# Performance work log

Hardware: AMD Instinct MI355X
Metric: run time of the kernel (lower is better)

The kernel has to match this reference:

```python
import jax, jax.numpy as jnp
import numpy as np

B, N, E, T, DIN, H, G, ND, NT, L = 4, 10000, 320000, 16, 16, 64, 64, 16, 3, 7


def _mlp2(x, W1, b1, W2, b2):
    # Linear -> LeakyReLU -> (Dropout: eval identity) -> Linear -> LeakyReLU
    h = jax.nn.leaky_relu(x @ W1 + b1)
    return jax.nn.leaky_relu(h @ W2 + b2)


def _gcn_conv(x, src, dst, ew, nt, W1, b1, W2, b2):
    # x: [B,N,D], nt: [B,N,ND], ew: [*,E,1] broadcastable over batch
    x_in = _mlp2(jnp.concatenate([x, nt], axis=-1), W1, b1, W2, b2)  # [B,N,G]
    msgs = x_in[:, src, :] * ew                                      # gather + weight, [B,E,G]
    aggr = jnp.zeros(x_in.shape, x_in.dtype).at[:, dst, :].add(msgs) # scatter-add, [B,N,G]
    return x + aggr


def _gru(x, Wx, Wh, bx, bh):
    # PyTorch-style GRU over time axis. x: [B,N,T,DIN] -> hs: [T,B,N,H]
    xw = jnp.einsum('bntd,dh->tbnh', x, Wx) + bx  # precompute input projections [T,B,N,3H]
    h0 = jnp.zeros(x.shape[:2] + (Wh.shape[0],), x.dtype)

    def step(h, xw_t):
        hw = h @ Wh + bh
        xr, xz, xn = jnp.split(xw_t, 3, axis=-1)
        hr, hz, hn = jnp.split(hw, 3, axis=-1)
        r = jax.nn.sigmoid(xr + hr)
        z = jax.nn.sigmoid(xz + hz)
        n = jnp.tanh(xn + r * hn)
        h_new = (1 - z) * n + z * h
        return h_new, h_new

    _, hs = jax.lax.scan(step, h0, xw)
    return hs


def reference(input_day, edge_attr, gru_Wx, gru_Wh, gru_bx, gru_bh,
              rnn_fc_W, rnn_fc_b,
              e_emb, e_c0_W1, e_c0_b1, e_c0_W2, e_c0_b2,
              e_c1_W1, e_c1_b1, e_c1_W2, e_c1_b2,
              e_fm_W1, e_fm_b1, e_fm_W2, e_fm_b2,
              g_emb, g_c0_W1, g_c0_b1, g_c0_W2, g_c0_b2,
              g_c1_W1, g_c1_b1, g_c1_W2, g_c1_b2,
              gcn_fc_W, gcn_fc_b,
              edge_index, node_type_ids):
    src, dst = edge_index[0], edge_index[1]

    # KRNN encoder (GRU) + max over time + FC head
    hs = _gru(input_day, gru_Wx, gru_Wh, gru_bx, gru_bh)  # [T,B,N,H]
    rnn_out = hs.max(axis=0)                              # kr_out.max(dim=-2) -> [B,N,H]
    y_rnn = rnn_out @ rnn_fc_W + rnn_fc_b                 # [B,N,L]

    # EdgeNet: GCN stack on static edge_attr, then per-edge pair MLP -> gate
    nt_e = jnp.broadcast_to(e_emb[node_type_ids][None], (B, N, ND))
    ew0 = edge_attr.reshape(1, E, 1)
    x = rnn_out
    x = _gcn_conv(x, src, dst, ew0, nt_e, e_c0_W1, e_c0_b1, e_c0_W2, e_c0_b2)
    x = _gcn_conv(x, src, dst, ew0, nt_e, e_c1_W1, e_c1_b1, e_c1_W2, e_c1_b2)
    edge_x = jnp.concatenate([x[:, src, :], x[:, dst, :]], axis=-1)  # [B,E,2G]
    h = jax.nn.leaky_relu(edge_x @ e_fm_W1 + e_fm_b1)
    edge_gate = jax.nn.relu(h @ e_fm_W2 + e_fm_b2)                   # [B,E,1]

    # Main GCNNet with learned edge gates
    nt_g = jnp.broadcast_to(g_emb[node_type_ids][None], (B, N, ND))
    x = rnn_out
    x = _gcn_conv(x, src, dst, edge_gate, nt_g, g_c0_W1, g_c0_b1, g_c0_W2, g_c0_b2)
    x = _gcn_conv(x, src, dst, edge_gate, nt_g, g_c1_W1, g_c1_b1, g_c1_W2, g_c1_b2)
    y_gcn = x @ gcn_fc_W + gcn_fc_b                                  # [B,N,L]

    return y_rnn + y_gcn


def setup_inputs() -> dict:
    key = jax.random.key(0)
    ks = iter(jax.random.split(key, 48))

    def nrm(shape, s=0.1):
        return jax.random.normal(next(ks), shape, jnp.float32) * s

    inp = {}
    inp['input_day'] = jax.random.normal(next(ks), (B, N, T, DIN), jnp.float32)
    inp['edge_index'] = jax.random.randint(next(ks), (2, E), 0, N)
    inp['node_type_ids'] = jax.random.randint(next(ks), (N,), 0, NT)
    inp['edge_attr'] = jax.random.uniform(next(ks), (E,), jnp.float32)

    inp['gru_Wx'] = nrm((DIN, 3 * H))
    inp['gru_Wh'] = nrm((H, 3 * H))
    inp['gru_bx'] = jnp.zeros((3 * H,), jnp.float32)
    inp['gru_bh'] = jnp.zeros((3 * H,), jnp.float32)
    inp['rnn_fc_W'] = nrm((H, L))
    inp['rnn_fc_b'] = jnp.zeros((L,), jnp.float32)

    inp['e_emb'] = nrm((NT, ND))
    inp['g_emb'] = nrm((NT, ND))
    for pre, in_dim in (('e_c0', H + ND), ('e_c1', G + ND), ('g_c0', H + ND), ('g_c1', G + ND)):
        inp[pre + '_W1'] = nrm((in_dim, G))
        inp[pre + '_b1'] = jnp.zeros((G,), jnp.float32)
        inp[pre + '_W2'] = nrm((G, G))
        inp[pre + '_b2'] = jnp.zeros((G,), jnp.float32)

    inp['e_fm_W1'] = nrm((2 * G, G))
    inp['e_fm_b1'] = jnp.zeros((G,), jnp.float32)
    inp['e_fm_W2'] = nrm((G, 1))
    inp['e_fm_b2'] = jnp.zeros((1,), jnp.float32)

    inp['gcn_fc_W'] = nrm((G, L))
    inp['gcn_fc_b'] = jnp.zeros((L,), jnp.float32)
    return inp
```

## Files before the change

kernel.cpp:

```cpp
#include <hip/hip_runtime.h>
#include <hip/hip_bf16.h>

#define NB 4
#define NN 10000
#define NE 320000
#define BN 40000
#define NL 7

typedef float f32x4 __attribute__((ext_vector_type(4)));
typedef __bf16 bf16x8 __attribute__((ext_vector_type(8)));

__device__ __forceinline__ float bf2f(unsigned short u){
  unsigned x = ((unsigned)u) << 16;
  return __builtin_bit_cast(float, x);
}
__device__ __forceinline__ unsigned short f2bf(float f){
  unsigned u = __builtin_bit_cast(unsigned, f);
  u += 0x7fffu + ((u >> 16) & 1u);
  return (unsigned short)(u >> 16);
}
__device__ __forceinline__ __bf16 f2b(float f){
  return __builtin_bit_cast(__bf16, f2bf(f));
}
__device__ __forceinline__ bf16x8 zero8(){
  uint4 z = make_uint4(0u,0u,0u,0u);
  return __builtin_bit_cast(bf16x8, z);
}
__device__ __forceinline__ bf16x8 ld8bf(const unsigned short* p){
  uint4 u = *(const uint4*)p;
  return __builtin_bit_cast(bf16x8, u);
}
__device__ __forceinline__ bf16x8 ld8f(const float* p){
  float4 a = *(const float4*)p;
  float4 b = *(const float4*)(p+4);
  bf16x8 r;
  r[0]=f2b(a.x); r[1]=f2b(a.y); r[2]=f2b(a.z); r[3]=f2b(a.w);
  r[4]=f2b(b.x); r[5]=f2b(b.y); r[6]=f2b(b.z); r[7]=f2b(b.w);
  return r;
}
__device__ __forceinline__ float frcp(float x){ return __builtin_amdgcn_rcpf(x); }
__device__ __forceinline__ float sigm(float x){ return frcp(1.f+__expf(-x)); }
__device__ __forceinline__ float tanh_(float x){ return 1.f - 2.f*frcp(__expf(2.f*x)+1.f); }
__device__ __forceinline__ float lrelu(float x){ return x > 0.f ? x : 0.01f*x; }

#define LDS_WAIT() asm volatile("s_waitcnt lgkmcnt(0)" ::: "memory")

__global__ __launch_bounds__(256, 2) void gru_kernel(
    const float* __restrict__ xd,
    const float* __restrict__ Wx,
    const float* __restrict__ Wh,
    const float* __restrict__ bx,
    const float* __restrict__ bh,
    float* __restrict__ rnn)
{
  __shared__ __attribute__((aligned(16))) unsigned short WhT[192][72];
  __shared__ __attribute__((aligned(16))) unsigned short WxT[192][40];
  __shared__ __attribute__((aligned(16))) unsigned short hb[4][16][72];
  int tid = threadIdx.x;
  int wave = tid >> 6, lane = tid & 63;
  int ln16 = lane & 15, quad = lane >> 4;

  for (int i = tid; i < 64*192; i += 256){
    int k = i / 192, n = i - k*192;
    WhT[n][k] = f2bf(Wh[i]);
  }
  for (int i = tid; i < 16*192; i += 256){
    int k = i / 192, n = i - k*192;
    WxT[n][k] = f2bf(Wx[i]);
    WxT[n][16+k] = 0;
  }
  for (int i = tid; i < 4*16*72; i += 256) ((unsigned short*)hb)[i] = 0;
  __syncthreads();

  int rowbase = blockIdx.x * 64 + wave * 16;

  bf16x8 whf[2][12];
  #pragma unroll
  for (int kt=0; kt<2; ++kt)
    #pragma unroll
    for (int nt=0; nt<12; ++nt)
      whf[kt][nt] = ld8bf(&WhT[nt*16 + ln16][kt*32 + quad*8]);

  float br_[4], bz_[4], bxn_[4], bhn_[4];
  #pragma unroll
  for (int j=0;j<4;++j){
    br_[j]  = bx[j*16+ln16]     + bh[j*16+ln16];
    bz_[j]  = bx[(4+j)*16+ln16] + bh[(4+j)*16+ln16];
    bxn_[j] = bx[(8+j)*16+ln16];
    bhn_[j] = bh[(8+j)*16+ln16];
  }

  f32x4 hprev[4], vmax[4];
  #pragma unroll
  for (int j=0;j<4;++j){
    hprev[j] = (f32x4){0.f,0.f,0.f,0.f};
    vmax[j]  = (f32x4){-1e30f,-1e30f,-1e30f,-1e30f};
  }

  const float* xrow = xd + (size_t)(rowbase + ln16) * 256;
  unsigned short* hrow = &hb[wave][ln16][0];

  bf16x8 axc = (quad < 2) ? ld8f(xrow + quad*8) : zero8();

  for (int t = 0; t < 16; ++t){
    bf16x8 axn = (t < 15 && quad < 2) ? ld8f(xrow + (t+1)*16 + quad*8) : zero8();
    bf16x8 ah0 = ld8bf(hrow + quad*8);
    bf16x8 ah1 = ld8bf(hrow + 32 + quad*8);

    #pragma unroll
    for (int j=0;j<4;++j){
      bf16x8 xr = ld8bf(&WxT[j*16+ln16][quad*8]);
      bf16x8 xz = ld8bf(&WxT[(4+j)*16+ln16][quad*8]);
      bf16x8 xn = ld8bf(&WxT[(8+j)*16+ln16][quad*8]);
      f32x4 ar = (f32x4){br_[j],br_[j],br_[j],br_[j]};
      ar = __builtin_amdgcn_mfma_f32_16x16x32_bf16(axc, xr, ar, 0,0,0);
      ar = __builtin_amdgcn_mfma_f32_16x16x32_bf16(ah0, whf[0][j], ar, 0,0,0);
      ar = __builtin_amdgcn_mfma_f32_16x16x32_bf16(ah1, whf[1][j], ar, 0,0,0);
      f32x4 az = (f32x4){bz_[j],bz_[j],bz_[j],bz_[j]};
      az = __builtin_amdgcn_mfma_f32_16x16x32_bf16(axc, xz, az, 0,0,0);
      az = __builtin_amdgcn_mfma_f32_16x16x32_bf16(ah0, whf[0][4+j], az, 0,0,0);
      az = __builtin_amdgcn_mfma_f32_16x16x32_bf16(ah1, whf[1][4+j], az, 0,0,0);
      f32x4 an = (f32x4){bxn_[j],bxn_[j],bxn_[j],bxn_[j]};
      an = __builtin_amdgcn_mfma_f32_16x16x32_bf16(axc, xn, an, 0,0,0);
      f32x4 ah = (f32x4){bhn_[j],bhn_[j],bhn_[j],bhn_[j]};
      ah = __builtin_amdgcn_mfma_f32_16x16x32_bf16(ah0, whf[0][8+j], ah, 0,0,0);
      ah = __builtin_amdgcn_mfma_f32_16x16x32_bf16(ah1, whf[1][8+j], ah, 0,0,0);
      #pragma unroll
      for (int i=0;i<4;++i){
        float r  = sigm(ar[i]);
        float z  = sigm(az[i]);
        float nn = tanh_(an[i] + r * ah[i]);
        float h  = fmaf(z, hprev[j][i]-nn, nn);
        hprev[j][i] = h;
        vmax[j][i] = fmaxf(vmax[j][i], h);
        hb[wave][quad*4+i][j*16+ln16] = f2bf(h);
      }
    }
    LDS_WAIT();
    axc = axn;
  }
  #pragma unroll
  for (int j=0;j<4;++j)
    #pragma unroll
    for (int i=0;i<4;++i)
      rnn[(size_t)(rowbase + quad*4 + i)*64 + j*16 + ln16] = vmax[j][i];
}

__global__ __launch_bounds__(256, 2) void mlp2_kernel(
    const float* __restrict__ x,
    const int* __restrict__ ntid,
    const float* __restrict__ emb,
    const float* __restrict__ W1,
    const float* __restrict__ b1,
    const float* __restrict__ W2,
    const float* __restrict__ b2,
    unsigned short* __restrict__ out)
{
  __shared__ __attribute__((aligned(16))) unsigned short W1T[64][96];
  __shared__ __attribute__((aligned(16))) unsigned short W2T[64][72];
  __shared__ __attribute__((aligned(16))) unsigned short hb[4][16][72];
  __shared__ float sb1[64], sb2[64];
  int tid = threadIdx.x;
  for (int i=tid;i<80*64;i+=256){ int k=i>>6, n=i&63; W1T[n][k]=f2bf(W1[i]); }
  for (int i=tid;i<64*16;i+=256){ int n=i>>4, k=80+(i&15); W1T[n][k]=0; }
  for (int i=tid;i<64*64;i+=256){ int k=i>>6, n=i&63; W2T[n][k]=f2bf(W2[i]); }
  if (tid<64){ sb1[tid]=b1[tid]; sb2[tid]=b2[tid]; }
  __syncthreads();

  int wave = tid>>6, lane = tid&63, ln16 = lane&15, quad = lane>>4;
  int row0 = blockIdx.x*64 + wave*16;
  int r_ = row0 + ln16;
  const float* xr = x + (size_t)r_*64;
  bf16x8 a0 = ld8f(xr + quad*8);
  bf16x8 a1 = ld8f(xr + 32 + quad*8);
  int id = ntid[r_ % NN];
  bf16x8 a2 = (quad<2) ? ld8f(emb + id*16 + quad*8) : zero8();

  f32x4 acc[4];
  #pragma unroll
  for (int nt=0;nt<4;++nt){
    float bb = sb1[nt*16+ln16];
    acc[nt] = (f32x4){bb,bb,bb,bb};
    acc[nt] = __builtin_amdgcn_mfma_f32_16x16x32_bf16(a0, ld8bf(&W1T[nt*16+ln16][quad*8]),    acc[nt], 0,0,0);
    acc[nt] = __builtin_amdgcn_mfma_f32_16x16x32_bf16(a1, ld8bf(&W1T[nt*16+ln16][32+quad*8]), acc[nt], 0,0,0);
    acc[nt] = __builtin_amdgcn_mfma_f32_16x16x32_bf16(a2, ld8bf(&W1T[nt*16+ln16][64+quad*8]), acc[nt], 0,0,0);
  }
  #pragma unroll
  for (int nt=0;nt<4;++nt)
    #pragma unroll
    for (int i=0;i<4;++i)
      hb[wave][quad*4+i][nt*16+ln16] = f2bf(lrelu(acc[nt][i]));
  LDS_WAIT();
  bf16x8 h0 = ld8bf(&hb[wave][ln16][quad*8]);
  bf16x8 h1 = ld8bf(&hb[wave][ln16][32+quad*8]);
  f32x4 acc2[4];
  #pragma unroll
  for (int nt=0;nt<4;++nt){
    float bb = sb2[nt*16+ln16];
    acc2[nt] = (f32x4){bb,bb,bb,bb};
    acc2[nt] = __builtin_amdgcn_mfma_f32_16x16x32_bf16(h0, ld8bf(&W2T[nt*16+ln16][quad*8]),    acc2[nt], 0,0,0);
    acc2[nt] = __builtin_amdgcn_mfma_f32_16x16x32_bf16(h1, ld8bf(&W2T[nt*16+ln16][32+quad*8]), acc2[nt], 0,0,0);
  }
  #pragma unroll
  for (int nt=0;nt<4;++nt)
    #pragma unroll
    for (int i=0;i<4;++i)
      out[(size_t)(row0+quad*4+i)*64 + nt*16+ln16] = f2bf(lrelu(acc2[nt][i]));
}

__global__ __launch_bounds__(256, 2) void uv_kernel(
    const float* __restrict__ x,
    const float* __restrict__ W1,
    unsigned short* __restrict__ uvp)
{
  __shared__ __attribute__((aligned(16))) unsigned short WT[128][72];
  int tid=threadIdx.x;
  for (int i=tid;i<64*64;i+=256){
    int k=i>>6, n=i&63;
    WT[n][k]    = f2bf(W1[i]);
    WT[64+n][k] = f2bf(W1[64*64 + i]);
  }
  __syncthreads();
  int wave=tid>>6, lane=tid&63, ln16=lane&15, quad=lane>>4;
  int row0 = blockIdx.x*64 + wave*16;
  const float* xr = x + (size_t)(row0+ln16)*64;
  bf16x8 a0 = ld8f(xr + quad*8);
  bf16x8 a1 = ld8f(xr + 32 + quad*8);
  f32x4 acc[8];
  #pragma unroll
  for (int nt=0;nt<8;++nt){
    acc[nt] = (f32x4){0.f,0.f,0.f,0.f};
    acc[nt] = __builtin_amdgcn_mfma_f32_16x16x32_bf16(a0, ld8bf(&WT[nt*16+ln16][quad*8]),    acc[nt], 0,0,0);
    acc[nt] = __builtin_amdgcn_mfma_f32_16x16x32_bf16(a1, ld8bf(&WT[nt*16+ln16][32+quad*8]), acc[nt], 0,0,0);
  }
  #pragma unroll
  for (int nt=0;nt<8;++nt)
    #pragma unroll
    for (int i=0;i<4;++i)
      uvp[(size_t)(row0+quad*4+i)*128 + nt*16+ln16] = f2bf(acc[nt][i]);
}

__global__ __launch_bounds__(256) void count_kernel(const int* __restrict__ ei, int* __restrict__ counts){
  int e = blockIdx.x*256+threadIdx.x;
  atomicAdd(&counts[ei[NE+e]], 1);
}
__global__ __launch_bounds__(1024) void scan_kernel(const int* __restrict__ counts,
                                                    int* __restrict__ rowptr, int* __restrict__ cursor){
  __shared__ int wsum[16];
  __shared__ int carrysh;
  int tid=threadIdx.x, wave=tid>>6, lane=tid&63;
  if (tid==0) carrysh=0;
  __syncthreads();
  for (int base=0;base<NN;base+=1024){
    int i=base+tid;
    int v = (i<NN)? counts[i] : 0;
    int s = v;
    #pragma unroll
    for (int off=1;off<64;off<<=1){
      int t_ = __shfl_up(s, off);
      if (lane>=off) s += t_;
    }
    if (lane==63) wsum[wave]=s;
    __syncthreads();
    if (wave==0){
      int w_ = (lane<16)? wsum[lane]:0;
      #pragma unroll
      for (int off=1;off<16;off<<=1){
        int t_ = __shfl_up(w_, off);
        if (lane>=off) w_ += t_;
      }
      if (lane<16) wsum[lane]=w_;
    }
    __syncthreads();
    int woff = (wave>0)? wsum[wave-1] : 0;
    int c = carrysh;
    int excl = s + woff + c - v;
    if (i<NN){ rowptr[i]=excl; cursor[i]=excl; }
    __syncthreads();
    if (tid==0) carrysh = c + wsum[15];
    __syncthreads();
  }
  if (tid==0) rowptr[NN]=carrysh;
}
__global__ __launch_bounds__(256) void fill_kernel(const int* __restrict__ ei,
                                                   const float* __restrict__ ea,
                                                   int* __restrict__ cursor,
                                                   int* __restrict__ ssrc,
                                                   float* __restrict__ wcsr){
  int e = blockIdx.x*256+threadIdx.x;
  int d = ei[NE+e];
  int pos = atomicAdd(&cursor[d],1);
  ssrc[pos]=ei[e];
  wcsr[pos]=ea[e];
}

__global__ __launch_bounds__(64) void aggr_kernel(
    const float* x,
    const unsigned short* __restrict__ xin,
    const int* __restrict__ rowptr,
    const int* __restrict__ ssrc,
    const float* __restrict__ wp,
    int bstride,
    float* out)
{
  int lane=threadIdx.x;
  int sub=lane>>4, l=lane&15;
  int bid = blockIdx.x;
  int b = bid / NN, n = bid - b*NN;
  int p0 = rowptr[n], p1 = rowptr[n+1];
  const unsigned short* xb_ = xin + (size_t)b*NN*64;
  const float* wb = wp + (size_t)b*bstride;
  float a0=0.f, a1=0.f, a2=0.f, a3=0.f;
  for (int p=p0+sub; p<p1; p+=4){
    int s = ssrc[p];
    float w = wb[p];
    uint2 m = *(const uint2*)(xb_ + (size_t)s*64 + l*4);
    a0 += bf2f((unsigned short)(m.x & 0xffffu)) * w;
    a1 += bf2f((unsigned short)(m.x >> 16)) * w;
    a2 += bf2f((unsigned short)(m.y & 0xffffu)) * w;
    a3 += bf2f((unsigned short)(m.y >> 16)) * w;
  }
  a0 += __shfl_xor(a0,16); a0 += __shfl_xor(a0,32);
  a1 += __shfl_xor(a1,16); a1 += __shfl_xor(a1,32);
  a2 += __shfl_xor(a2,16); a2 += __shfl_xor(a2,32);
  a3 += __shfl_xor(a3,16); a3 += __shfl_xor(a3,32);
  if (sub==0){
    float4 base = *(const float4*)(x + (size_t)bid*64 + l*4);
    float4 o; o.x=base.x+a0; o.y=base.y+a1; o.z=base.z+a2; o.w=base.w+a3;
    *(float4*)(out + (size_t)bid*64 + l*4) = o;
  }
}

__global__ __launch_bounds__(64) void gate_kernel(
    const unsigned short* __restrict__ uvp,
    const int* __restrict__ rowptr,
    const int* __restrict__ ssrc,
    const float* __restrict__ b1,
    const float* __restrict__ W2,
    const float* __restrict__ b2,
    float* __restrict__ gate)
{
  int lane=threadIdx.x;
  int sub=lane>>4, l=lane&15;
  int bid = blockIdx.x;
  int b = bid / NN, n = bid - b*NN;
  int p0 = rowptr[n], p1 = rowptr[n+1];
  const unsigned short* ub = uvp + (size_t)b*NN*128;
  uint2 vu = *(const uint2*)(ub + (size_t)n*128 + 64 + l*4);
  float v0=bf2f((unsigned short)(vu.x&0xffffu)), v1=bf2f((unsigned short)(vu.x>>16));
  float v2=bf2f((unsigned short)(vu.y&0xffffu)), v3=bf2f((unsigned short)(vu.y>>16));
  float4 bb = *(const float4*)(b1 + l*4);
  float4 ww = *(const float4*)(W2 + l*4);
  float b2v = b2[0];
  float* gb = gate + (size_t)b*NE;
  for (int p=p0+sub; p<p1; p+=4){
    int s = ssrc[p];
    uint2 uu = *(const uint2*)(ub + (size_t)s*128 + l*4);
    float h0 = lrelu(bf2f((unsigned short)(uu.x&0xffffu)) + v0 + bb.x);
    float h1 = lrelu(bf2f((unsigned short)(uu.x>>16))     + v1 + bb.y);
    float h2 = lrelu(bf2f((unsigned short)(uu.y&0xffffu)) + v2 + bb.z);
    float h3 = lrelu(bf2f((unsigned short)(uu.y>>16))     + v3 + bb.w);
    float part = h0*ww.x + h1*ww.y + h2*ww.z + h3*ww.w;
    part += __shfl_xor(part,1);
    part += __shfl_xor(part,2);
    part += __shfl_xor(part,4);
    part += __shfl_xor(part,8);
    if (l==0){
      float g = part + b2v;
      gb[p] = g>0.f ? g : 0.f;
    }
  }
}

__global__ __launch_bounds__(256) void final_kernel(
    const float* __restrict__ rnn, const float* __restrict__ xg,
    const float* __restrict__ Wr, const float* __restrict__ br,
    const float* __restrict__ Wg, const float* __restrict__ bg,
    float* __restrict__ out)
{
  __shared__ float sWr[64*7], sWg[64*7], sbr[7], sbg[7];
  int tid=threadIdx.x;
  for (int i=tid;i<448;i+=256){ sWr[i]=Wr[i]; sWg[i]=Wg[i]; }
  if (tid<7){ sbr[tid]=br[tid]; sbg[tid]=bg[tid]; }
  __syncthreads();
  int row = blockIdx.x*256+tid;
  if (row>=BN) return;
  float acc[7];
  #pragma unroll
  for (int l=0;l<7;++l) acc[l]=sbr[l]+sbg[l];
  const float* rp = rnn + (size_t)row*64;
  const float* gp = xg  + (size_t)row*64;
  #pragma unroll 4
  for (int k4=0;k4<16;++k4){
    float4 a = *(const float4*)(rp + k4*4);
    float4 c = *(const float4*)(gp + k4*4);
    #pragma unroll
    for (int l=0;l<7;++l){
      acc[l] += a.x*sWr[(k4*4+0)*7+l] + a.y*sWr[(k4*4+1)*7+l]
              + a.z*sWr[(k4*4+2)*7+l] + a.w*sWr[(k4*4+3)*7+l]
              + c.x*sWg[(k4*4+0)*7+l] + c.y*sWg[(k4*4+1)*7+l]
              + c.z*sWg[(k4*4+2)*7+l] + c.w*sWg[(k4*4+3)*7+l];
    }
  }
  #pragma unroll
  for (int l=0;l<7;++l) out[(size_t)row*7+l] = acc[l];
}

extern "C" void kernel_launch(void* const* d_in, const int* in_sizes, int n_in,
                              void* d_out, int out_size, void* d_ws, size_t ws_size,
                              hipStream_t stream)
{
  (void)in_sizes; (void)n_in; (void)out_size; (void)ws_size;
  const float* input_day = (const float*)d_in[0];
  const int* ei    = (const int*)d_in[1];
  const int* ntid  = (const int*)d_in[2];
  const float* edge_attr = (const float*)d_in[3];
  const float* gWx = (const float*)d_in[4];
  const float* gWh = (const float*)d_in[5];
  const float* gbx = (const float*)d_in[6];
  const float* gbh = (const float*)d_in[7];
  const float* rW  = (const float*)d_in[8];
  const float* rb  = (const float*)d_in[9];
  const float* eemb= (const float*)d_in[10];
  const float* gemb= (const float*)d_in[11];
  const float* ec0W1=(const float*)d_in[12];
  const float* ec0b1=(const float*)d_in[13];
  const float* ec0W2=(const float*)d_in[14];
  const float* ec0b2=(const float*)d_in[15];
  const float* ec1W1=(const float*)d_in[16];
  const float* ec1b1=(const float*)d_in[17];
  const float* ec1W2=(const float*)d_in[18];
  const float* ec1b2=(const float*)d_in[19];
  const float* gc0W1=(const float*)d_in[20];
  const float* gc0b1=(const float*)d_in[21];
  const float* gc0W2=(const float*)d_in[22];
  const float* gc0b2=(const float*)d_in[23];
  const float* gc1W1=(const float*)d_in[24];
  const float* gc1b1=(const float*)d_in[25];
  const float* gc1W2=(const float*)d_in[26];
  const float* gc1b2=(const float*)d_in[27];
  const float* efmW1=(const float*)d_in[28];
  const float* efmb1=(const float*)d_in[29];
  const float* efmW2=(const float*)d_in[30];
  const float* efmb2=(const float*)d_in[31];
  const float* gcnW =(const float*)d_in[32];
  const float* gcnb =(const float*)d_in[33];

  char* ws = (char*)d_ws;
  float*          rnn = (float*)(ws);
  float*          xe  = (float*)(ws + 10240000);
  unsigned short* xin = (unsigned short*)(ws + 20480000);
  unsigned short* uvp = (unsigned short*)(ws + 25600000);
  float*          gat = (float*)(ws + 35840000);
  int* rowptr= (int*)(ws + 40960000);
  int* cursor= (int*)(ws + 41000064);
  int* counts= (int*)(ws + 41040064);
  int*   ssrc= (int*)(ws + 41080064);
  float* wcsr= (float*)(ws + 42360064);

  hipMemsetAsync(counts, 0, NN*sizeof(int), stream);
  count_kernel<<<NE/256, 256, 0, stream>>>(ei, counts);
  scan_kernel<<<1, 1024, 0, stream>>>(counts, rowptr, cursor);
  fill_kernel<<<NE/256, 256, 0, stream>>>(ei, edge_attr, cursor, ssrc, wcsr);

  gru_kernel<<<625, 256, 0, stream>>>(input_day, gWx, gWh, gbx, gbh, rnn);

  mlp2_kernel<<<625, 256, 0, stream>>>(rnn, ntid, eemb, ec0W1, ec0b1, ec0W2, ec0b2, xin);
  aggr_kernel<<<BN, 64, 0, stream>>>(rnn, xin, rowptr, ssrc, wcsr, 0, xe);
  mlp2_kernel<<<625, 256, 0, stream>>>(xe, ntid, eemb, ec1W1, ec1b1, ec1W2, ec1b2, xin);
  aggr_kernel<<<BN, 64, 0, stream>>>(xe, xin, rowptr, ssrc, wcsr, 0, xe);

  uv_kernel<<<625, 256, 0, stream>>>(xe, efmW1, uvp);
  gate_kernel<<<BN, 64, 0, stream>>>(uvp, rowptr, ssrc, efmb1, efmW2, efmb2, gat);

  mlp2_kernel<<<625, 256, 0, stream>>>(rnn, ntid, gemb, gc0W1, gc0b1, gc0W2, gc0b2, xin);
  aggr_kernel<<<BN, 64, 0, stream>>>(rnn, xin, rowptr, ssrc, gat, NE, xe);
  mlp2_kernel<<<625, 256, 0, stream>>>(xe, ntid, gemb, gc1W1, gc1b1, gc1W2, gc1b2, xin);
  aggr_kernel<<<BN, 64, 0, stream>>>(xe, xin, rowptr, ssrc, gat, NE, xe);

  final_kernel<<<(BN+255)/256, 256, 0, stream>>>(rnn, xe, rW, rb, gcnW, gcnb,
                                                 (float*)d_out);
}
```

Baseline: 499.2 us.

## Pack aggregation waves per block, fuse final head, parallelize scan, hoist Wx fragments

Several independent changes. The aggregation and gate kernels now run four waves per 256-thread block instead of one wave per block, with unroll-2 edge loops. The last aggregation is fused with the final linear head, which removes the final_kernel launch and one global round trip. The single-block scan now gives each wave a contiguous 640-element chunk and synchronises only twice, where before it synchronised on every 1024-element pass. The GRU keeps its Wx fragments in registers across timesteps instead of reloading them from LDS each step, at the cost of more register pressure.

```diff
diff --git a/kernel.cpp b/kernel.cpp
--- a/kernel.cpp
+++ b/kernel.cpp
@@ -81,6 +81,11 @@
     for (int nt=0; nt<12; ++nt)
       whf[kt][nt] = ld8bf(&WhT[nt*16 + ln16][kt*32 + quad*8]);
 
+  bf16x8 wxf[12];
+  #pragma unroll
+  for (int nt=0; nt<12; ++nt)
+    wxf[nt] = ld8bf(&WxT[nt*16 + ln16][quad*8]);
+
   float br_[4], bz_[4], bxn_[4], bhn_[4];
   #pragma unroll
   for (int j=0;j<4;++j){
@@ -109,19 +114,16 @@
 
     #pragma unroll
     for (int j=0;j<4;++j){
-      bf16x8 xr = ld8bf(&WxT[j*16+ln16][quad*8]);
-      bf16x8 xz = ld8bf(&WxT[(4+j)*16+ln16][quad*8]);
-      bf16x8 xn = ld8bf(&WxT[(8+j)*16+ln16][quad*8]);
       f32x4 ar = (f32x4){br_[j],br_[j],br_[j],br_[j]};
-      ar = __builtin_amdgcn_mfma_f32_16x16x32_bf16(axc, xr, ar, 0,0,0);
+      ar = __builtin_amdgcn_mfma_f32_16x16x32_bf16(axc, wxf[j], ar, 0,0,0);
       ar = __builtin_amdgcn_mfma_f32_16x16x32_bf16(ah0, whf[0][j], ar, 0,0,0);
       ar = __builtin_amdgcn_mfma_f32_16x16x32_bf16(ah1, whf[1][j], ar, 0,0,0);
       f32x4 az = (f32x4){bz_[j],bz_[j],bz_[j],bz_[j]};
-      az = __builtin_amdgcn_mfma_f32_16x16x32_bf16(axc, xz, az, 0,0,0);
+      az = __builtin_amdgcn_mfma_f32_16x16x32_bf16(axc, wxf[4+j], az, 0,0,0);
       az = __builtin_amdgcn_mfma_f32_16x16x32_bf16(ah0, whf[0][4+j], az, 0,0,0);
       az = __builtin_amdgcn_mfma_f32_16x16x32_bf16(ah1, whf[1][4+j], az, 0,0,0);
       f32x4 an = (f32x4){bxn_[j],bxn_[j],bxn_[j],bxn_[j]};
-      an = __builtin_amdgcn_mfma_f32_16x16x32_bf16(axc, xn, an, 0,0,0);
+      an = __builtin_amdgcn_mfma_f32_16x16x32_bf16(axc, wxf[8+j], an, 0,0,0);
       f32x4 ah = (f32x4){bhn_[j],bhn_[j],bhn_[j],bhn_[j]};
       ah = __builtin_amdgcn_mfma_f32_16x16x32_bf16(ah0, whf[0][8+j], ah, 0,0,0);
       ah = __builtin_amdgcn_mfma_f32_16x16x32_bf16(ah1, whf[1][8+j], ah, 0,0,0);
@@ -246,13 +248,14 @@
 }
 __global__ __launch_bounds__(1024) void scan_kernel(const int* __restrict__ counts,
                                                     int* __restrict__ rowptr, int* __restrict__ cursor){
+  __shared__ int incl[10240];
   __shared__ int wsum[16];
-  __shared__ int carrysh;
   int tid=threadIdx.x, wave=tid>>6, lane=tid&63;
-  if (tid==0) carrysh=0;
-  __syncthreads();
-  for (int base=0;base<NN;base+=1024){
-    int i=base+tid;
+  int base = wave*640;
+  int carry=0;
+  #pragma unroll
+  for (int c=0;c<10;++c){
+    int i = base + c*64 + lane;
     int v = (i<NN)? counts[i] : 0;
     int s = v;
     #pragma unroll
@@ -260,27 +263,32 @@
       int t_ = __shfl_up(s, off);
       if (lane>=off) s += t_;
     }
-    if (lane==63) wsum[wave]=s;
-    __syncthreads();
-    if (wave==0){
-      int w_ = (lane<16)? wsum[lane]:0;
-      #pragma unroll
-      for (int off=1;off<16;off<<=1){
-        int t_ = __shfl_up(w_, off);
-        if (lane>=off) w_ += t_;
-      }
-      if (lane<16) wsum[lane]=w_;
-    }
-    __syncthreads();
-    int woff = (wave>0)? wsum[wave-1] : 0;
-    int c = carrysh;
-    int excl = s + woff + c - v;
-    if (i<NN){ rowptr[i]=excl; cursor[i]=excl; }
-    __syncthreads();
-    if (tid==0) carrysh = c + wsum[15];
-    __syncthreads();
-  }
-  if (tid==0) rowptr[NN]=carrysh;
+    s += carry;
+    incl[base + c*64 + lane] = s;
+    carry = __shfl(s, 63);
+  }
+  if (lane==63) wsum[wave]=carry;
+  __syncthreads();
+  if (wave==0){
+    int w_ = (lane<16)? wsum[lane]:0;
+    #pragma unroll
+    for (int off=1;off<16;off<<=1){
+      int t_ = __shfl_up(w_, off);
+      if (lane>=off) w_ += t_;
+    }
+    if (lane<16) wsum[lane]=w_;
+  }
+  __syncthreads();
+  int woff = (wave>0)? wsum[wave-1] : 0;
+  #pragma unroll
+  for (int c=0;c<10;++c){
+    int i = base + c*64 + lane;
+    if (i<NN){
+      int excl = incl[i] + woff - counts[i];
+      rowptr[i]=excl; cursor[i]=excl;
+    }
+  }
+  if (tid==0) rowptr[NN]=wsum[15];
 }
 __global__ __launch_bounds__(256) void fill_kernel(const int* __restrict__ ei,
                                                    const float* __restrict__ ea,
@@ -294,7 +302,7 @@
   wcsr[pos]=ea[e];
 }
 
-__global__ __launch_bounds__(64) void aggr_kernel(
+__global__ __launch_bounds__(256) void aggr_kernel(
     const float* x,
     const unsigned short* __restrict__ xin,
     const int* __restrict__ rowptr,
@@ -303,14 +311,16 @@
     int bstride,
     float* out)
 {
-  int lane=threadIdx.x;
+  int tid=threadIdx.x;
+  int wave=tid>>6, lane=tid&63;
   int sub=lane>>4, l=lane&15;
-  int bid = blockIdx.x;
+  int bid = blockIdx.x*4 + wave;
   int b = bid / NN, n = bid - b*NN;
   int p0 = rowptr[n], p1 = rowptr[n+1];
   const unsigned short* xb_ = xin + (size_t)b*NN*64;
   const float* wb = wp + (size_t)b*bstride;
   float a0=0.f, a1=0.f, a2=0.f, a3=0.f;
+  #pragma unroll 2
   for (int p=p0+sub; p<p1; p+=4){
     int s = ssrc[p];
     float w = wb[p];
@@ -331,7 +341,70 @@
   }
 }
 
-__global__ __launch_bounds__(64) void gate_kernel(
+__global__ __launch_bounds__(256) void aggr_final_kernel(
+    const float* x,
+    const unsigned short* __restrict__ xin,
+    const int* __restrict__ rowptr,
+    const int* __restrict__ ssrc,
+    const float* __restrict__ wp,
+    const float* __restrict__ rnn,
+    const float* __restrict__ Wr, const float* __restrict__ br,
+    const float* __restrict__ Wg, const float* __restrict__ bg,
+    float* __restrict__ out)
+{
+  __shared__ float sWr[448], sWg[448], sb[7];
+  int tid=threadIdx.x;
+  for (int i=tid;i<448;i+=256){ sWr[i]=Wr[i]; sWg[i]=Wg[i]; }
+  if (tid<7) sb[tid]=br[tid]+bg[tid];
+  __syncthreads();
+  int wave=tid>>6, lane=tid&63;
+  int sub=lane>>4, l=lane&15;
+  int bid = blockIdx.x*4 + wave;
+  int b = bid / NN, n = bid - b*NN;
+  int p0 = rowptr[n], p1 = rowptr[n+1];
+  const unsigned short* xb_ = xin + (size_t)b*NN*64;
+  const float* wb = wp + (size_t)b*NE;
+  float a0=0.f, a1=0.f, a2=0.f, a3=0.f;
+  #pragma unroll 2
+  for (int p=p0+sub; p<p1; p+=4){
+    int s = ssrc[p];
+    float w = wb[p];
+    uint2 m = *(const uint2*)(xb_ + (size_t)s*64 + l*4);
+    a0 += bf2f((unsigned short)(m.x & 0xffffu)) * w;
+    a1 += bf2f((unsigned short)(m.x >> 16)) * w;
+    a2 += bf2f((unsigned short)(m.y & 0xffffu)) * w;
+    a3 += bf2f((unsigned short)(m.y >> 16)) * w;
+  }
+  a0 += __shfl_xor(a0,16); a0 += __shfl_xor(a0,32);
+  a1 += __shfl_xor(a1,16); a1 += __shfl_xor(a1,32);
+  a2 += __shfl_xor(a2,16); a2 += __shfl_xor(a2,32);
+  a3 += __shfl_xor(a3,16); a3 += __shfl_xor(a3,32);
+  if (sub==0){
+    float4 base = *(const float4*)(x + (size_t)bid*64 + l*4);
+    float o0=base.x+a0, o1=base.y+a1, o2=base.z+a2, o3=base.w+a3;
+    float4 rr = *(const float4*)(rnn + (size_t)bid*64 + l*4);
+    float part[7];
+    #pragma unroll
+    for (int q=0;q<7;++q)
+      part[q] = o0*sWg[(l*4+0)*7+q] + o1*sWg[(l*4+1)*7+q]
+              + o2*sWg[(l*4+2)*7+q] + o3*sWg[(l*4+3)*7+q]
+              + rr.x*sWr[(l*4+0)*7+q] + rr.y*sWr[(l*4+1)*7+q]
+              + rr.z*sWr[(l*4+2)*7+q] + rr.w*sWr[(l*4+3)*7+q];
+    #pragma unroll
+    for (int q=0;q<7;++q){
+      part[q] += __shfl_xor(part[q],1);
+      part[q] += __shfl_xor(part[q],2);
+      part[q] += __shfl_xor(part[q],4);
+      part[q] += __shfl_xor(part[q],8);
+    }
+    if (l==0){
+      #pragma unroll
+      for (int q=0;q<7;++q) out[(size_t)bid*7+q] = part[q] + sb[q];
+    }
+  }
+}
+
+__global__ __launch_bounds__(256) void gate_kernel(
     const unsigned short* __restrict__ uvp,
     const int* __restrict__ rowptr,
     const int* __restrict__ ssrc,
@@ -340,9 +413,10 @@
     const float* __restrict__ b2,
     float* __restrict__ gate)
 {
-  int lane=threadIdx.x;
+  int tid=threadIdx.x;
+  int wave=tid>>6, lane=tid&63;
   int sub=lane>>4, l=lane&15;
-  int bid = blockIdx.x;
+  int bid = blockIdx.x*4 + wave;
   int b = bid / NN, n = bid - b*NN;
   int p0 = rowptr[n], p1 = rowptr[n+1];
   const unsigned short* ub = uvp + (size_t)b*NN*128;
@@ -353,6 +427,7 @@
   float4 ww = *(const float4*)(W2 + l*4);
   float b2v = b2[0];
   float* gb = gate + (size_t)b*NE;
+  #pragma unroll 2
   for (int p=p0+sub; p<p1; p+=4){
     int s = ssrc[p];
     uint2 uu = *(const uint2*)(ub + (size_t)s*128 + l*4);
@@ -370,40 +445,6 @@
       gb[p] = g>0.f ? g : 0.f;
     }
   }
-}
-
-__global__ __launch_bounds__(256) void final_kernel(
-    const float* __restrict__ rnn, const float* __restrict__ xg,
-    const float* __restrict__ Wr, const float* __restrict__ br,
-    const float* __restrict__ Wg, const float* __restrict__ bg,
-    float* __restrict__ out)
-{
-  __shared__ float sWr[64*7], sWg[64*7], sbr[7], sbg[7];
-  int tid=threadIdx.x;
-  for (int i=tid;i<448;i+=256){ sWr[i]=Wr[i]; sWg[i]=Wg[i]; }
-  if (tid<7){ sbr[tid]=br[tid]; sbg[tid]=bg[tid]; }
-  __syncthreads();
-  int row = blockIdx.x*256+tid;
-  if (row>=BN) return;
-  float acc[7];
-  #pragma unroll
-  for (int l=0;l<7;++l) acc[l]=sbr[l]+sbg[l];
-  const float* rp = rnn + (size_t)row*64;
-  const float* gp = xg  + (size_t)row*64;
-  #pragma unroll 4
-  for (int k4=0;k4<16;++k4){
-    float4 a = *(const float4*)(rp + k4*4);
-    float4 c = *(const float4*)(gp + k4*4);
-    #pragma unroll
-    for (int l=0;l<7;++l){
-      acc[l] += a.x*sWr[(k4*4+0)*7+l] + a.y*sWr[(k4*4+1)*7+l]
-              + a.z*sWr[(k4*4+2)*7+l] + a.w*sWr[(k4*4+3)*7+l]
-              + c.x*sWg[(k4*4+0)*7+l] + c.y*sWg[(k4*4+1)*7+l]
-              + c.z*sWg[(k4*4+2)*7+l] + c.w*sWg[(k4*4+3)*7+l];
-    }
-  }
-  #pragma unroll
-  for (int l=0;l<7;++l) out[(size_t)row*7+l] = acc[l];
 }
 
 extern "C" void kernel_launch(void* const* d_in, const int* in_sizes, int n_in,
@@ -466,18 +507,16 @@
   gru_kernel<<<625, 256, 0, stream>>>(input_day, gWx, gWh, gbx, gbh, rnn);
 
   mlp2_kernel<<<625, 256, 0, stream>>>(rnn, ntid, eemb, ec0W1, ec0b1, ec0W2, ec0b2, xin);
-  aggr_kernel<<<BN, 64, 0, stream>>>(rnn, xin, rowptr, ssrc, wcsr, 0, xe);
+  aggr_kernel<<<BN/4, 256, 0, stream>>>(rnn, xin, rowptr, ssrc, wcsr, 0, xe);
   mlp2_kernel<<<625, 256, 0, stream>>>(xe, ntid, eemb, ec1W1, ec1b1, ec1W2, ec1b2, xin);
-  aggr_kernel<<<BN, 64, 0, stream>>>(xe, xin, rowptr, ssrc, wcsr, 0, xe);
+  aggr_kernel<<<BN/4, 256, 0, stream>>>(xe, xin, rowptr, ssrc, wcsr, 0, xe);
 
   uv_kernel<<<625, 256, 0, stream>>>(xe, efmW1, uvp);
-  gate_kernel<<<BN, 64, 0, stream>>>(uvp, rowptr, ssrc, efmb1, efmW2, efmb2, gat);
+  gate_kernel<<<BN/4, 256, 0, stream>>>(uvp, rowptr, ssrc, efmb1, efmW2, efmb2, gat);
 
   mlp2_kernel<<<625, 256, 0, stream>>>(rnn, ntid, gemb, gc0W1, gc0b1, gc0W2, gc0b2, xin);
-  aggr_kernel<<<BN, 64, 0, stream>>>(rnn, xin, rowptr, ssrc, gat, NE, xe);
+  aggr_kernel<<<BN/4, 256, 0, stream>>>(rnn, xin, rowptr, ssrc, gat, NE, xe);
   mlp2_kernel<<<625, 256, 0, stream>>>(xe, ntid, gemb, gc1W1, gc1b1, gc1W2, gc1b2, xin);
-  aggr_kernel<<<BN, 64, 0, stream>>>(xe, xin, rowptr, ssrc, gat, NE, xe);
-
-  final_kernel<<<(BN+255)/256, 256, 0, stream>>>(rnn, xe, rW, rb, gcnW, gcnb,
-                                                 (float*)d_out);
-}
+  aggr_final_kernel<<<BN/4, 256, 0, stream>>>(xe, xin, rowptr, ssrc, gat, rnn,
+                                              rW, rb, gcnW, gcnb, (float*)d_out);
+}
```

New measurement: 501.2 us. No clear change (+0.4%).
